# Kernel optimization log

Measured on AMD Instinct MI355X. Metric: run time of the kernel, lower is better.

Reference implementation:

```python
import jax, jax.numpy as jnp
import numpy as np

B, T, C = 4, 2048, 1024
H, D = 16, 64


def setup_inputs() -> dict:
    key = jax.random.key(0)
    ks = jax.random.split(key, 6)
    s = 0.02
    return {
        "x": jax.random.normal(ks[0], (B, T, C), dtype=jnp.float32),
        "wq": jax.random.normal(ks[1], (H, C, D), dtype=jnp.float32) * s,
        "wk": jax.random.normal(ks[2], (H, C, D), dtype=jnp.float32) * s,
        "wv": jax.random.normal(ks[3], (H, C, D), dtype=jnp.float32) * s,
        "w_proj": jax.random.normal(ks[4], (C, C), dtype=jnp.float32) * s,
        "b_proj": jnp.zeros((C,), dtype=jnp.float32),
    }


def reference(x, wq, wk, wv, w_proj, b_proj):
    b, t, c = x.shape
    # per-head projections, vectorized over heads: [B,T,C] x [H,C,D] -> [B,H,T,D]
    q = jnp.einsum("btc,hcd->bhtd", x, wq)
    k = jnp.einsum("btc,hcd->bhtd", x, wk)
    v = jnp.einsum("btc,hcd->bhtd", x, wv)
    # NOTE: original scales by C**-0.5 where C = n_embd (not head_size)
    scale = jnp.asarray(c, x.dtype) ** -0.5
    scores = jnp.einsum("bhtd,bhsd->bhts", q, k) * scale  # [B,H,T,T]
    causal = jnp.tril(jnp.ones((t, t), dtype=bool))
    scores = jnp.where(causal, scores, jnp.finfo(x.dtype).min)
    wei = jax.nn.softmax(scores, axis=-1)
    out = jnp.einsum("bhts,bhsd->bhtd", wei, v)  # [B,H,T,D]
    out = out.transpose(0, 2, 1, 3).reshape(b, t, c)  # concat heads
    return out @ w_proj + b_proj
```

## Files before the change

### kernel.cpp

```cpp
#include <hip/hip_runtime.h>
#include <hip/hip_bf16.h>
#include <stdint.h>

#define B_ 4
#define T_ 2048
#define C_ 1024
#define H_ 16
#define D_ 64

typedef __attribute__((ext_vector_type(8))) short bf16x8;
typedef __attribute__((ext_vector_type(4))) float f32x4;

static __device__ __forceinline__ short f2bf(float f) {
    union { float f; unsigned u; } v; v.f = f;
    unsigned r = v.u + 0x7fffu + ((v.u >> 16) & 1u);
    return (short)(r >> 16);
}

#define GLD_LDS16(g, l) __builtin_amdgcn_global_load_lds( \
    (const __attribute__((address_space(1))) void*)(g),   \
    (__attribute__((address_space(3))) void*)(l), 16, 0, 0)

__global__ void pack_x(const float* __restrict__ x, short* __restrict__ xb) {
    int t = blockIdx.x * blockDim.x + threadIdx.x;
    const float* src = x + (size_t)t * 8;
    float4 v0 = *(const float4*)src;
    float4 v1 = *(const float4*)(src + 4);
    bf16x8 o;
    o[0] = f2bf(v0.x); o[1] = f2bf(v0.y); o[2] = f2bf(v0.z); o[3] = f2bf(v0.w);
    o[4] = f2bf(v1.x); o[5] = f2bf(v1.y); o[6] = f2bf(v1.z); o[7] = f2bf(v1.w);
    *(bf16x8*)(xb + (size_t)t * 8) = o;
}

__global__ void pack_wqkv(const float* __restrict__ wq, const float* __restrict__ wk,
                          const float* __restrict__ wv, short* __restrict__ out) {
    int tid = blockIdx.x * blockDim.x + threadIdx.x;
    int n  = tid >> 7;
    int kc = tid & 127;
    int qkv = n >> 10;
    int h = (n >> 6) & 15;
    int d = n & 63;
    const float* w = (qkv == 0) ? wq : (qkv == 1) ? wk : wv;
    const float* src = w + (size_t)h * (C_ * D_) + d;
    short* dst = out + (size_t)n * C_ + kc * 8;
#pragma unroll
    for (int j = 0; j < 8; ++j)
        dst[j] = f2bf(src[(size_t)(kc * 8 + j) * D_]);
}

__global__ void pack_wproj(const float* __restrict__ wp, short* __restrict__ out) {
    int tid = blockIdx.x * blockDim.x + threadIdx.x;
    int n  = tid >> 7;
    int kc = tid & 127;
    short* dst = out + (size_t)n * C_ + kc * 8;
#pragma unroll
    for (int j = 0; j < 8; ++j)
        dst[j] = f2bf(wp[(size_t)(kc * 8 + j) * C_ + n]);
}

template<bool OUT_F32>
__global__ __launch_bounds__(256)
void gemm_lds(const short* __restrict__ A, const short* __restrict__ Bt,
              void* __restrict__ Cptr, const float* __restrict__ bias,
              int M, int N, int K) {
    __shared__ short As[128 * 32];
    __shared__ short Bs[128 * 32];
    const int tid = threadIdx.x;
    const int lane = tid & 63, wid = tid >> 6;
    const int wr = wid >> 1, wc = wid & 1;
    const int l15 = lane & 15, l4 = lane >> 4;
    const int m0 = blockIdx.y * 128, n0 = blockIdx.x * 128;

    f32x4 acc[4][4] = {};

    for (int k0 = 0; k0 < K; k0 += 32) {
#pragma unroll
        for (int p = 0; p < 2; ++p) {
            int e = p * 256 + tid;
            int r = e >> 2, c = e & 3;
            GLD_LDS16(A  + (size_t)(m0 + r) * K + k0 + c * 8, As + e * 8);
            GLD_LDS16(Bt + (size_t)(n0 + r) * K + k0 + c * 8, Bs + e * 8);
        }
        __syncthreads();
        bf16x8 af[4], bfr[4];
#pragma unroll
        for (int m = 0; m < 4; ++m)
            af[m] = *(const bf16x8*)(As + (wr * 64 + m * 16 + l15) * 32 + l4 * 8);
#pragma unroll
        for (int n = 0; n < 4; ++n)
            bfr[n] = *(const bf16x8*)(Bs + (wc * 64 + n * 16 + l15) * 32 + l4 * 8);
#pragma unroll
        for (int m = 0; m < 4; ++m)
#pragma unroll
            for (int n = 0; n < 4; ++n)
                acc[m][n] = __builtin_amdgcn_mfma_f32_16x16x32_bf16(af[m], bfr[n], acc[m][n], 0, 0, 0);
        __syncthreads();
    }

#pragma unroll
    for (int m = 0; m < 4; ++m) {
        int row_base = m0 + wr * 64 + m * 16 + l4 * 4;
#pragma unroll
        for (int n = 0; n < 4; ++n) {
            int col = n0 + wc * 64 + n * 16 + l15;
#pragma unroll
            for (int r = 0; r < 4; ++r) {
                int row = row_base + r;
                float v = acc[m][n][r];
                if (OUT_F32) {
                    ((float*)Cptr)[(size_t)row * N + col] = v + (bias ? bias[col] : 0.0f);
                } else {
                    ((short*)Cptr)[(size_t)row * N + col] = f2bf(v);
                }
            }
        }
    }
}

__device__ __forceinline__ void softmax_pv_phase1(
    f32x4 S[4], f32x4 O[4], float* mrow, float* srow,
    int qrow0, int s0, bool diag, int l15, int l4, short* ps) {
    float pmax[4];
#pragma unroll
    for (int r = 0; r < 4; ++r) pmax[r] = -1e30f;
#pragma unroll
    for (int n = 0; n < 4; ++n) {
#pragma unroll
        for (int r = 0; r < 4; ++r) {
            float v = S[n][r] * 0.03125f;
            if (diag) {
                int scol = s0 + n * 16 + l15;
                if (scol > qrow0 + r) v = -1e30f;
            }
            S[n][r] = v;
            pmax[r] = fmaxf(pmax[r], v);
        }
    }
#pragma unroll
    for (int r = 0; r < 4; ++r) {
        float v = pmax[r];
        v = fmaxf(v, __shfl_xor(v, 1));
        v = fmaxf(v, __shfl_xor(v, 2));
        v = fmaxf(v, __shfl_xor(v, 4));
        v = fmaxf(v, __shfl_xor(v, 8));
        pmax[r] = v;
    }
    float psum[4];
#pragma unroll
    for (int r = 0; r < 4; ++r) {
        float mnew = fmaxf(mrow[r], pmax[r]);
        float fr = __expf(mrow[r] - mnew);
        mrow[r] = mnew;
        srow[r] *= fr;
#pragma unroll
        for (int n = 0; n < 4; ++n) O[n][r] *= fr;
        psum[r] = 0.0f;
    }
#pragma unroll
    for (int n = 0; n < 4; ++n) {
#pragma unroll
        for (int r = 0; r < 4; ++r) {
            float p = __expf(S[n][r] - mrow[r]);
            psum[r] += p;
            ps[(l4 * 4 + r) * 72 + n * 16 + l15] = f2bf(p);
        }
    }
#pragma unroll
    for (int r = 0; r < 4; ++r) {
        float v = psum[r];
        v += __shfl_xor(v, 1);
        v += __shfl_xor(v, 2);
        v += __shfl_xor(v, 4);
        v += __shfl_xor(v, 8);
        srow[r] += v;
    }
}

__global__ __launch_bounds__(256)
void attn_v5(const short* __restrict__ qkv, short* __restrict__ out) {
    const int pi = blockIdx.x;
    const int bh = blockIdx.y;
    const int b = bh >> 4;
    const int h = bh & 15;
    const int qA0 = pi * 64;
    const int qB0 = (31 - pi) * 64;
    const int ntA = pi + 1;
    const int ntB = 32 - pi;
    const int tid = threadIdx.x;
    const int wave = tid >> 6;
    const int lane = tid & 63;
    const int l15 = lane & 15, l4 = lane >> 4;

    __shared__ short Vt[64][72];
    __shared__ short Ps[4][2][16][72];

    const size_t rs = 3 * C_;
    const short* qbA = qkv + ((size_t)b * T_ + qA0) * rs + h * 64;
    const short* qbB = qkv + ((size_t)b * T_ + qB0) * rs + h * 64;
    const short* kb  = qkv + (size_t)b * T_ * rs + C_ + h * 64;
    const short* vb  = qkv + (size_t)b * T_ * rs + 2 * C_ + h * 64;

    bf16x8 aqA0 = *(const bf16x8*)(qbA + (size_t)(wave * 16 + l15) * rs + l4 * 8);
    bf16x8 aqA1 = *(const bf16x8*)(qbA + (size_t)(wave * 16 + l15) * rs + 32 + l4 * 8);
    bf16x8 aqB0 = *(const bf16x8*)(qbB + (size_t)(wave * 16 + l15) * rs + l4 * 8);
    bf16x8 aqB1 = *(const bf16x8*)(qbB + (size_t)(wave * 16 + l15) * rs + 32 + l4 * 8);

    f32x4 OA[4] = {}, OB[4] = {};
    float mA[4], sA[4], mB[4], sB[4];
#pragma unroll
    for (int r = 0; r < 4; ++r) { mA[r] = mB[r] = -1e30f; sA[r] = sB[r] = 0.0f; }

    short* psB = &Ps[wave][0][0][0];
    short* psA = &Ps[wave][1][0][0];

    for (int t = 0; t < ntB; ++t) {
        const int s0 = t * 64;
        const bool actA = (t < ntA);
        __syncthreads();

#pragma unroll
        for (int p = 0; p < 2; ++p) {
            int e = p * 256 + tid;
            int d = e & 63, sc = e >> 6;
            bf16x8 v;
#pragma unroll
            for (int j = 0; j < 8; ++j)
                v[j] = vb[(size_t)(s0 + sc * 8 + j) * rs + d];
            *(bf16x8*)&Vt[d][sc * 8] = v;
        }

        bf16x8 bk0[4], bk1[4];
#pragma unroll
        for (int n = 0; n < 4; ++n) {
            const short* kr = kb + (size_t)(s0 + n * 16 + l15) * rs;
            bk0[n] = *(const bf16x8*)(kr + l4 * 8);
            bk1[n] = *(const bf16x8*)(kr + 32 + l4 * 8);
        }

        f32x4 S[4];
#pragma unroll
        for (int n = 0; n < 4; ++n) {
            f32x4 z = {};
            z = __builtin_amdgcn_mfma_f32_16x16x32_bf16(aqB0, bk0[n], z, 0, 0, 0);
            S[n] = __builtin_amdgcn_mfma_f32_16x16x32_bf16(aqB1, bk1[n], z, 0, 0, 0);
        }
        softmax_pv_phase1(S, OB, mB, sB, qB0 + wave * 16 + l4 * 4, s0,
                          s0 == qB0, l15, l4, psB);

        if (actA) {
            f32x4 SA[4];
#pragma unroll
            for (int n = 0; n < 4; ++n) {
                f32x4 z = {};
                z = __builtin_amdgcn_mfma_f32_16x16x32_bf16(aqA0, bk0[n], z, 0, 0, 0);
                SA[n] = __builtin_amdgcn_mfma_f32_16x16x32_bf16(aqA1, bk1[n], z, 0, 0, 0);
            }
            softmax_pv_phase1(SA, OA, mA, sA, qA0 + wave * 16 + l4 * 4, s0,
                              s0 == qA0, l15, l4, psA);
        }

        __syncthreads();

        bf16x8 apB0 = *(const bf16x8*)(psB + l15 * 72 + l4 * 8);
        bf16x8 apB1 = *(const bf16x8*)(psB + l15 * 72 + 32 + l4 * 8);
#pragma unroll
        for (int n = 0; n < 4; ++n) {
            bf16x8 bv0 = *(const bf16x8*)&Vt[n * 16 + l15][l4 * 8];
            bf16x8 bv1 = *(const bf16x8*)&Vt[n * 16 + l15][32 + l4 * 8];
            OB[n] = __builtin_amdgcn_mfma_f32_16x16x32_bf16(apB0, bv0, OB[n], 0, 0, 0);
            OB[n] = __builtin_amdgcn_mfma_f32_16x16x32_bf16(apB1, bv1, OB[n], 0, 0, 0);
        }
        if (actA) {
            bf16x8 apA0 = *(const bf16x8*)(psA + l15 * 72 + l4 * 8);
            bf16x8 apA1 = *(const bf16x8*)(psA + l15 * 72 + 32 + l4 * 8);
#pragma unroll
            for (int n = 0; n < 4; ++n) {
                bf16x8 bv0 = *(const bf16x8*)&Vt[n * 16 + l15][l4 * 8];
                bf16x8 bv1 = *(const bf16x8*)&Vt[n * 16 + l15][32 + l4 * 8];
                OA[n] = __builtin_amdgcn_mfma_f32_16x16x32_bf16(apA0, bv0, OA[n], 0, 0, 0);
                OA[n] = __builtin_amdgcn_mfma_f32_16x16x32_bf16(apA1, bv1, OA[n], 0, 0, 0);
            }
        }
    }

#pragma unroll
    for (int r = 0; r < 4; ++r) {
        int rowB = qB0 + wave * 16 + l4 * 4 + r;
        int rowA = qA0 + wave * 16 + l4 * 4 + r;
        float invB = 1.0f / sB[r];
        float invA = 1.0f / sA[r];
        size_t obB = ((size_t)b * T_ + rowB) * C_ + h * 64;
        size_t obA = ((size_t)b * T_ + rowA) * C_ + h * 64;
#pragma unroll
        for (int n = 0; n < 4; ++n) {
            out[obB + n * 16 + l15] = f2bf(OB[n][r] * invB);
            out[obA + n * 16 + l15] = f2bf(OA[n][r] * invA);
        }
    }
}

extern "C" void kernel_launch(void* const* d_in, const int* in_sizes, int n_in,
                              void* d_out, int out_size, void* d_ws, size_t ws_size,
                              hipStream_t stream) {
    const float* x     = (const float*)d_in[0];
    const float* wq    = (const float*)d_in[1];
    const float* wk    = (const float*)d_in[2];
    const float* wv    = (const float*)d_in[3];
    const float* wproj = (const float*)d_in[4];
    const float* bproj = (const float*)d_in[5];
    float* out = (float*)d_out;

    short* wqkv_t  = (short*)d_ws;
    short* wproj_t = wqkv_t + 3072 * 1024;
    short* qkv_b   = wproj_t + 1024 * 1024;
    short* attn_b  = qkv_b + (size_t)8192 * 3072;
    short* xb      = attn_b;

    pack_x<<<4096, 256, 0, stream>>>(x, xb);
    pack_wqkv<<<1536, 256, 0, stream>>>(wq, wk, wv, wqkv_t);
    pack_wproj<<<512, 256, 0, stream>>>(wproj, wproj_t);

    gemm_lds<false><<<dim3(24, 64), 256, 0, stream>>>(
        xb, wqkv_t, qkv_b, nullptr, 8192, 3072, 1024);

    attn_v5<<<dim3(16, 64), 256, 0, stream>>>(qkv_b, attn_b);

    gemm_lds<true><<<dim3(8, 64), 256, 0, stream>>>(
        attn_b, wproj_t, out, bproj, 8192, 1024, 1024);
}
```

Measured before the change: 321.7 us.

## Emit V transposed from QKV GEMM epilogue and drop LDS V staging

The QKV GEMM epilogue now writes Q and K into a 2048-wide buffer and writes V pre-transposed as [B*H, D, T], so the attention kernel can load V fragments directly from global memory into registers. This removes the per-tile scalar strided gather of V into LDS and both block-wide __syncthreads per tile, replacing them with a wave-local lgkmcnt wait since each wave only reads its own P tile. The P buffer row pitch also changes from 72 to 76 to alter LDS bank mapping. The trade-off is a strided transposed store in the GEMM epilogue and more global loads in flight per wave.

New measurement: 371.6 us. +15.5%, slower.

```diff
diff --git a/kernel.cpp b/kernel.cpp
--- a/kernel.cpp
+++ b/kernel.cpp
@@ -9,6 +9,7 @@
 #define D_ 64
 
 typedef __attribute__((ext_vector_type(8))) short bf16x8;
+typedef __attribute__((ext_vector_type(4))) short short4v;
 typedef __attribute__((ext_vector_type(4))) float f32x4;
 
 static __device__ __forceinline__ short f2bf(float f) {
@@ -58,11 +59,11 @@
         dst[j] = f2bf(wp[(size_t)(kc * 8 + j) * C_ + n]);
 }
 
-template<bool OUT_F32>
+template<int MODE>
 __global__ __launch_bounds__(256)
 void gemm_lds(const short* __restrict__ A, const short* __restrict__ Bt,
-              void* __restrict__ Cptr, const float* __restrict__ bias,
-              int M, int N, int K) {
+              void* __restrict__ Cptr, short* __restrict__ vtptr,
+              const float* __restrict__ bias, int M, int N, int K) {
     __shared__ short As[128 * 32];
     __shared__ short Bs[128 * 32];
     const int tid = threadIdx.x;
@@ -103,21 +104,30 @@
 #pragma unroll
         for (int n = 0; n < 4; ++n) {
             int col = n0 + wc * 64 + n * 16 + l15;
-#pragma unroll
-            for (int r = 0; r < 4; ++r) {
-                int row = row_base + r;
-                float v = acc[m][n][r];
-                if (OUT_F32) {
-                    ((float*)Cptr)[(size_t)row * N + col] = v + (bias ? bias[col] : 0.0f);
+            if (MODE == 1) {
+#pragma unroll
+                for (int r = 0; r < 4; ++r)
+                    ((float*)Cptr)[(size_t)(row_base + r) * N + col] =
+                        acc[m][n][r] + bias[col];
+            } else {
+                if (n0 < 2048) {
+#pragma unroll
+                    for (int r = 0; r < 4; ++r)
+                        ((short*)Cptr)[(size_t)(row_base + r) * 2048 + col] = f2bf(acc[m][n][r]);
                 } else {
-                    ((short*)Cptr)[(size_t)row * N + col] = f2bf(v);
+                    int cm = col - 2048;
+                    int bq = row_base >> 11, t = row_base & 2047;
+                    short4v s;
+                    s[0] = f2bf(acc[m][n][0]); s[1] = f2bf(acc[m][n][1]);
+                    s[2] = f2bf(acc[m][n][2]); s[3] = f2bf(acc[m][n][3]);
+                    *(short4v*)(vtptr + ((size_t)bq * 1024 + cm) * 2048 + t) = s;
                 }
             }
         }
     }
 }
 
-__device__ __forceinline__ void softmax_pv_phase1(
+__device__ __forceinline__ void softmax_phase(
     f32x4 S[4], f32x4 O[4], float* mrow, float* srow,
     int qrow0, int s0, bool diag, int l15, int l4, short* ps) {
     float pmax[4];
@@ -162,7 +172,7 @@
         for (int r = 0; r < 4; ++r) {
             float p = __expf(S[n][r] - mrow[r]);
             psum[r] += p;
-            ps[(l4 * 4 + r) * 72 + n * 16 + l15] = f2bf(p);
+            ps[(l4 * 4 + r) * 76 + n * 16 + l15] = f2bf(p);
         }
     }
 #pragma unroll
@@ -177,7 +187,8 @@
 }
 
 __global__ __launch_bounds__(256)
-void attn_v5(const short* __restrict__ qkv, short* __restrict__ out) {
+void attn_v6(const short* __restrict__ qk, const short* __restrict__ vt,
+             short* __restrict__ out) {
     const int pi = blockIdx.x;
     const int bh = blockIdx.y;
     const int b = bh >> 4;
@@ -191,14 +202,13 @@
     const int lane = tid & 63;
     const int l15 = lane & 15, l4 = lane >> 4;
 
-    __shared__ short Vt[64][72];
-    __shared__ short Ps[4][2][16][72];
-
-    const size_t rs = 3 * C_;
-    const short* qbA = qkv + ((size_t)b * T_ + qA0) * rs + h * 64;
-    const short* qbB = qkv + ((size_t)b * T_ + qB0) * rs + h * 64;
-    const short* kb  = qkv + (size_t)b * T_ * rs + C_ + h * 64;
-    const short* vb  = qkv + (size_t)b * T_ * rs + 2 * C_ + h * 64;
+    __shared__ short Ps[4][2][16][76];
+
+    const size_t rs = 2 * C_;
+    const short* qbA = qk + ((size_t)b * T_ + qA0) * rs + h * 64;
+    const short* qbB = qk + ((size_t)b * T_ + qB0) * rs + h * 64;
+    const short* kb  = qk + (size_t)b * T_ * rs + C_ + h * 64;
+    const short* vtb = vt + (size_t)bh * 64 * T_;
 
     bf16x8 aqA0 = *(const bf16x8*)(qbA + (size_t)(wave * 16 + l15) * rs + l4 * 8);
     bf16x8 aqA1 = *(const bf16x8*)(qbA + (size_t)(wave * 16 + l15) * rs + 32 + l4 * 8);
@@ -216,18 +226,6 @@
     for (int t = 0; t < ntB; ++t) {
         const int s0 = t * 64;
         const bool actA = (t < ntA);
-        __syncthreads();
-
-#pragma unroll
-        for (int p = 0; p < 2; ++p) {
-            int e = p * 256 + tid;
-            int d = e & 63, sc = e >> 6;
-            bf16x8 v;
-#pragma unroll
-            for (int j = 0; j < 8; ++j)
-                v[j] = vb[(size_t)(s0 + sc * 8 + j) * rs + d];
-            *(bf16x8*)&Vt[d][sc * 8] = v;
-        }
 
         bf16x8 bk0[4], bk1[4];
 #pragma unroll
@@ -236,6 +234,13 @@
             bk0[n] = *(const bf16x8*)(kr + l4 * 8);
             bk1[n] = *(const bf16x8*)(kr + 32 + l4 * 8);
         }
+        bf16x8 bv0[4], bv1[4];
+#pragma unroll
+        for (int n = 0; n < 4; ++n) {
+            const short* vr = vtb + (size_t)(n * 16 + l15) * T_ + s0;
+            bv0[n] = *(const bf16x8*)(vr + l4 * 8);
+            bv1[n] = *(const bf16x8*)(vr + 32 + l4 * 8);
+        }
 
         f32x4 S[4];
 #pragma unroll
@@ -244,8 +249,8 @@
             z = __builtin_amdgcn_mfma_f32_16x16x32_bf16(aqB0, bk0[n], z, 0, 0, 0);
             S[n] = __builtin_amdgcn_mfma_f32_16x16x32_bf16(aqB1, bk1[n], z, 0, 0, 0);
         }
-        softmax_pv_phase1(S, OB, mB, sB, qB0 + wave * 16 + l4 * 4, s0,
-                          s0 == qB0, l15, l4, psB);
+        softmax_phase(S, OB, mB, sB, qB0 + wave * 16 + l4 * 4, s0, s0 == qB0,
+                      l15, l4, psB);
 
         if (actA) {
             f32x4 SA[4];
@@ -255,30 +260,27 @@
                 z = __builtin_amdgcn_mfma_f32_16x16x32_bf16(aqA0, bk0[n], z, 0, 0, 0);
                 SA[n] = __builtin_amdgcn_mfma_f32_16x16x32_bf16(aqA1, bk1[n], z, 0, 0, 0);
             }
-            softmax_pv_phase1(SA, OA, mA, sA, qA0 + wave * 16 + l4 * 4, s0,
-                              s0 == qA0, l15, l4, psA);
-        }
-
-        __syncthreads();
-
-        bf16x8 apB0 = *(const bf16x8*)(psB + l15 * 72 + l4 * 8);
-        bf16x8 apB1 = *(const bf16x8*)(psB + l15 * 72 + 32 + l4 * 8);
-#pragma unroll
-        for (int n = 0; n < 4; ++n) {
-            bf16x8 bv0 = *(const bf16x8*)&Vt[n * 16 + l15][l4 * 8];
-            bf16x8 bv1 = *(const bf16x8*)&Vt[n * 16 + l15][32 + l4 * 8];
-            OB[n] = __builtin_amdgcn_mfma_f32_16x16x32_bf16(apB0, bv0, OB[n], 0, 0, 0);
-            OB[n] = __builtin_amdgcn_mfma_f32_16x16x32_bf16(apB1, bv1, OB[n], 0, 0, 0);
+            softmax_phase(SA, OA, mA, sA, qA0 + wave * 16 + l4 * 4, s0, s0 == qA0,
+                          l15, l4, psA);
+        }
+
+        asm volatile("s_waitcnt lgkmcnt(0)" ::: "memory");
+        __builtin_amdgcn_sched_barrier(0);
+
+        bf16x8 apB0 = *(const bf16x8*)(psB + l15 * 76 + l4 * 8);
+        bf16x8 apB1 = *(const bf16x8*)(psB + l15 * 76 + 32 + l4 * 8);
+#pragma unroll
+        for (int n = 0; n < 4; ++n) {
+            OB[n] = __builtin_amdgcn_mfma_f32_16x16x32_bf16(apB0, bv0[n], OB[n], 0, 0, 0);
+            OB[n] = __builtin_amdgcn_mfma_f32_16x16x32_bf16(apB1, bv1[n], OB[n], 0, 0, 0);
         }
         if (actA) {
-            bf16x8 apA0 = *(const bf16x8*)(psA + l15 * 72 + l4 * 8);
-            bf16x8 apA1 = *(const bf16x8*)(psA + l15 * 72 + 32 + l4 * 8);
+            bf16x8 apA0 = *(const bf16x8*)(psA + l15 * 76 + l4 * 8);
+            bf16x8 apA1 = *(const bf16x8*)(psA + l15 * 76 + 32 + l4 * 8);
 #pragma unroll
             for (int n = 0; n < 4; ++n) {
-                bf16x8 bv0 = *(const bf16x8*)&Vt[n * 16 + l15][l4 * 8];
-                bf16x8 bv1 = *(const bf16x8*)&Vt[n * 16 + l15][32 + l4 * 8];
-                OA[n] = __builtin_amdgcn_mfma_f32_16x16x32_bf16(apA0, bv0, OA[n], 0, 0, 0);
-                OA[n] = __builtin_amdgcn_mfma_f32_16x16x32_bf16(apA1, bv1, OA[n], 0, 0, 0);
+                OA[n] = __builtin_amdgcn_mfma_f32_16x16x32_bf16(apA0, bv0[n], OA[n], 0, 0, 0);
+                OA[n] = __builtin_amdgcn_mfma_f32_16x16x32_bf16(apA1, bv1[n], OA[n], 0, 0, 0);
             }
         }
     }
@@ -312,19 +314,20 @@
 
     short* wqkv_t  = (short*)d_ws;
     short* wproj_t = wqkv_t + 3072 * 1024;
-    short* qkv_b   = wproj_t + 1024 * 1024;
-    short* attn_b  = qkv_b + (size_t)8192 * 3072;
+    short* qk_b    = wproj_t + 1024 * 1024;
+    short* vt_b    = qk_b + (size_t)8192 * 2048;
+    short* attn_b  = vt_b + (size_t)64 * 64 * 2048;
     short* xb      = attn_b;
 
     pack_x<<<4096, 256, 0, stream>>>(x, xb);
     pack_wqkv<<<1536, 256, 0, stream>>>(wq, wk, wv, wqkv_t);
     pack_wproj<<<512, 256, 0, stream>>>(wproj, wproj_t);
 
-    gemm_lds<false><<<dim3(24, 64), 256, 0, stream>>>(
-        xb, wqkv_t, qkv_b, nullptr, 8192, 3072, 1024);
-
-    attn_v5<<<dim3(16, 64), 256, 0, stream>>>(qkv_b, attn_b);
-
-    gemm_lds<true><<<dim3(8, 64), 256, 0, stream>>>(
-        attn_b, wproj_t, out, bproj, 8192, 1024, 1024);
-}
+    gemm_lds<2><<<dim3(24, 64), 256, 0, stream>>>(
+        xb, wqkv_t, qk_b, vt_b, nullptr, 8192, 3072, 1024);
+
+    attn_v6<<<dim3(16, 64), 256, 0, stream>>>(qk_b, vt_b, attn_b);
+
+    gemm_lds<1><<<dim3(8, 64), 256, 0, stream>>>(
+        attn_b, wproj_t, out, nullptr, bproj, 8192, 1024, 1024);
+}
```

## Double-buffer V tile with register prefetch and drop per-tile P barrier

Applied to the files above, without the earlier changes.

The V tile is now held in two LDS buffers. The next tile's V loads are issued into registers at the start of each iteration and stored into the other buffer after the softmax, so global latency overlaps the QK and softmax compute. Because P is per-wave, the second block barrier becomes a wave-local lgkmcnt wait. The transposed V store uses an XOR swizzle, the P row pitch changes to 76, and MFMA sections are wrapped in s_setprio. This costs more LDS and extra registers for the prefetched V and adds correctness sensitivity to the barrier removal.

Result: slower. 340.3 us (+5.8%).

```diff
diff --git a/kernel.cpp b/kernel.cpp
--- a/kernel.cpp
+++ b/kernel.cpp
@@ -117,7 +117,7 @@
     }
 }
 
-__device__ __forceinline__ void softmax_pv_phase1(
+__device__ __forceinline__ void softmax_phase(
     f32x4 S[4], f32x4 O[4], float* mrow, float* srow,
     int qrow0, int s0, bool diag, int l15, int l4, short* ps) {
     float pmax[4];
@@ -162,7 +162,7 @@
         for (int r = 0; r < 4; ++r) {
             float p = __expf(S[n][r] - mrow[r]);
             psum[r] += p;
-            ps[(l4 * 4 + r) * 72 + n * 16 + l15] = f2bf(p);
+            ps[(l4 * 4 + r) * 76 + n * 16 + l15] = f2bf(p);
         }
     }
 #pragma unroll
@@ -177,7 +177,7 @@
 }
 
 __global__ __launch_bounds__(256)
-void attn_v5(const short* __restrict__ qkv, short* __restrict__ out) {
+void attn_v8(const short* __restrict__ qkv, short* __restrict__ out) {
     const int pi = blockIdx.x;
     const int bh = blockIdx.y;
     const int b = bh >> 4;
@@ -191,8 +191,8 @@
     const int lane = tid & 63;
     const int l15 = lane & 15, l4 = lane >> 4;
 
-    __shared__ short Vt[64][72];
-    __shared__ short Ps[4][2][16][72];
+    __shared__ short Vt[2][64][64];
+    __shared__ short Ps[4][2][16][76];
 
     const size_t rs = 3 * C_;
     const short* qbA = qkv + ((size_t)b * T_ + qA0) * rs + h * 64;
@@ -213,20 +213,34 @@
     short* psB = &Ps[wave][0][0][0];
     short* psA = &Ps[wave][1][0][0];
 
+    const int vd = lane;
+    const int sc0 = wave, sc1 = 4 + wave;
+    const int pc0 = (sc0 ^ (vd & 7)) * 8;
+    const int pc1 = (sc1 ^ (vd & 7)) * 8;
+
+    bf16x8 vreg0, vreg1;
+#pragma unroll
+    for (int j = 0; j < 8; ++j) {
+        vreg0[j] = vb[(size_t)(sc0 * 8 + j) * rs + vd];
+        vreg1[j] = vb[(size_t)(sc1 * 8 + j) * rs + vd];
+    }
+    *(bf16x8*)&Vt[0][vd][pc0] = vreg0;
+    *(bf16x8*)&Vt[0][vd][pc1] = vreg1;
+
     for (int t = 0; t < ntB; ++t) {
         const int s0 = t * 64;
+        const int cur = t & 1;
         const bool actA = (t < ntA);
+        const bool pre = (t + 1 < ntB);
+
         __syncthreads();
 
-#pragma unroll
-        for (int p = 0; p < 2; ++p) {
-            int e = p * 256 + tid;
-            int d = e & 63, sc = e >> 6;
-            bf16x8 v;
-#pragma unroll
-            for (int j = 0; j < 8; ++j)
-                v[j] = vb[(size_t)(s0 + sc * 8 + j) * rs + d];
-            *(bf16x8*)&Vt[d][sc * 8] = v;
+        if (pre) {
+#pragma unroll
+            for (int j = 0; j < 8; ++j) {
+                vreg0[j] = vb[(size_t)(s0 + 64 + sc0 * 8 + j) * rs + vd];
+                vreg1[j] = vb[(size_t)(s0 + 64 + sc1 * 8 + j) * rs + vd];
+            }
         }
 
         bf16x8 bk0[4], bk1[4];
@@ -238,48 +252,64 @@
         }
 
         f32x4 S[4];
+        __builtin_amdgcn_s_setprio(1);
 #pragma unroll
         for (int n = 0; n < 4; ++n) {
             f32x4 z = {};
             z = __builtin_amdgcn_mfma_f32_16x16x32_bf16(aqB0, bk0[n], z, 0, 0, 0);
             S[n] = __builtin_amdgcn_mfma_f32_16x16x32_bf16(aqB1, bk1[n], z, 0, 0, 0);
         }
-        softmax_pv_phase1(S, OB, mB, sB, qB0 + wave * 16 + l4 * 4, s0,
-                          s0 == qB0, l15, l4, psB);
+        __builtin_amdgcn_s_setprio(0);
+        softmax_phase(S, OB, mB, sB, qB0 + wave * 16 + l4 * 4, s0, s0 == qB0,
+                      l15, l4, psB);
 
         if (actA) {
             f32x4 SA[4];
+            __builtin_amdgcn_s_setprio(1);
 #pragma unroll
             for (int n = 0; n < 4; ++n) {
                 f32x4 z = {};
                 z = __builtin_amdgcn_mfma_f32_16x16x32_bf16(aqA0, bk0[n], z, 0, 0, 0);
                 SA[n] = __builtin_amdgcn_mfma_f32_16x16x32_bf16(aqA1, bk1[n], z, 0, 0, 0);
             }
-            softmax_pv_phase1(SA, OA, mA, sA, qA0 + wave * 16 + l4 * 4, s0,
-                              s0 == qA0, l15, l4, psA);
-        }
-
-        __syncthreads();
-
-        bf16x8 apB0 = *(const bf16x8*)(psB + l15 * 72 + l4 * 8);
-        bf16x8 apB1 = *(const bf16x8*)(psB + l15 * 72 + 32 + l4 * 8);
-#pragma unroll
-        for (int n = 0; n < 4; ++n) {
-            bf16x8 bv0 = *(const bf16x8*)&Vt[n * 16 + l15][l4 * 8];
-            bf16x8 bv1 = *(const bf16x8*)&Vt[n * 16 + l15][32 + l4 * 8];
+            __builtin_amdgcn_s_setprio(0);
+            softmax_phase(SA, OA, mA, sA, qA0 + wave * 16 + l4 * 4, s0, s0 == qA0,
+                          l15, l4, psA);
+        }
+
+        if (pre) {
+            *(bf16x8*)&Vt[cur ^ 1][vd][pc0] = vreg0;
+            *(bf16x8*)&Vt[cur ^ 1][vd][pc1] = vreg1;
+        }
+
+        asm volatile("s_waitcnt lgkmcnt(0)" ::: "memory");
+        __builtin_amdgcn_sched_barrier(0);
+
+        bf16x8 apB0 = *(const bf16x8*)(psB + l15 * 76 + l4 * 8);
+        bf16x8 apB1 = *(const bf16x8*)(psB + l15 * 76 + 32 + l4 * 8);
+        __builtin_amdgcn_s_setprio(1);
+#pragma unroll
+        for (int n = 0; n < 4; ++n) {
+            const short* vrow = &Vt[cur][n * 16 + l15][0];
+            bf16x8 bv0 = *(const bf16x8*)(vrow + ((l4 ^ (l15 & 7)) * 8));
+            bf16x8 bv1 = *(const bf16x8*)(vrow + (((l4 + 4) ^ (l15 & 7)) * 8));
             OB[n] = __builtin_amdgcn_mfma_f32_16x16x32_bf16(apB0, bv0, OB[n], 0, 0, 0);
             OB[n] = __builtin_amdgcn_mfma_f32_16x16x32_bf16(apB1, bv1, OB[n], 0, 0, 0);
         }
+        __builtin_amdgcn_s_setprio(0);
         if (actA) {
-            bf16x8 apA0 = *(const bf16x8*)(psA + l15 * 72 + l4 * 8);
-            bf16x8 apA1 = *(const bf16x8*)(psA + l15 * 72 + 32 + l4 * 8);
+            bf16x8 apA0 = *(const bf16x8*)(psA + l15 * 76 + l4 * 8);
+            bf16x8 apA1 = *(const bf16x8*)(psA + l15 * 76 + 32 + l4 * 8);
+            __builtin_amdgcn_s_setprio(1);
 #pragma unroll
             for (int n = 0; n < 4; ++n) {
-                bf16x8 bv0 = *(const bf16x8*)&Vt[n * 16 + l15][l4 * 8];
-                bf16x8 bv1 = *(const bf16x8*)&Vt[n * 16 + l15][32 + l4 * 8];
+                const short* vrow = &Vt[cur][n * 16 + l15][0];
+                bf16x8 bv0 = *(const bf16x8*)(vrow + ((l4 ^ (l15 & 7)) * 8));
+                bf16x8 bv1 = *(const bf16x8*)(vrow + (((l4 + 4) ^ (l15 & 7)) * 8));
                 OA[n] = __builtin_amdgcn_mfma_f32_16x16x32_bf16(apA0, bv0, OA[n], 0, 0, 0);
                 OA[n] = __builtin_amdgcn_mfma_f32_16x16x32_bf16(apA1, bv1, OA[n], 0, 0, 0);
             }
+            __builtin_amdgcn_s_setprio(0);
         }
     }
 
@@ -323,7 +353,7 @@
     gemm_lds<false><<<dim3(24, 64), 256, 0, stream>>>(
         xb, wqkv_t, qkv_b, nullptr, 8192, 3072, 1024);
 
-    attn_v5<<<dim3(16, 64), 256, 0, stream>>>(qkv_b, attn_b);
+    attn_v8<<<dim3(16, 64), 256, 0, stream>>>(qkv_b, attn_b);
 
     gemm_lds<true><<<dim3(8, 64), 256, 0, stream>>>(
         attn_b, wproj_t, out, bproj, 8192, 1024, 1024);
```

## Fold softmax scale into Q projection, use exp2, lazy rescale, swizzle LDS

Applied to the files above, without the earlier changes.

The QKV GEMM epilogue now multiplies the Q columns by scale*log2(e), so the attention kernel can use raw v_exp_f32 (exp2) without a per-score multiply. The online softmax skips the running-max rescale of O and the row sum when the new block maximum stays within 8 units of the stored max across the wave. The Vt LDS tile uses an XOR swizzle in place of padding, and the P tile stride changes from 72 to 76, both aimed at reducing bank conflicts. The lazy rescale lets exponentials reach up to 2^8 before rescaling, which is safe in fp32 but slightly changes the rounding of bf16 P values.

After: 333.3 us. 1.04x slower.

```diff
diff --git a/kernel.cpp b/kernel.cpp
--- a/kernel.cpp
+++ b/kernel.cpp
@@ -17,9 +17,17 @@
     return (short)(r >> 16);
 }
 
+static __device__ __forceinline__ float fast_exp2(float x) {
+    float r;
+    asm("v_exp_f32 %0, %1" : "=v"(r) : "v"(x));
+    return r;
+}
+
 #define GLD_LDS16(g, l) __builtin_amdgcn_global_load_lds( \
     (const __attribute__((address_space(1))) void*)(g),   \
     (__attribute__((address_space(3))) void*)(l), 16, 0, 0)
+
+#define QSCALE 0.04508422f
 
 __global__ void pack_x(const float* __restrict__ x, short* __restrict__ xb) {
     int t = blockIdx.x * blockDim.x + threadIdx.x;
@@ -58,7 +66,7 @@
         dst[j] = f2bf(wp[(size_t)(kc * 8 + j) * C_ + n]);
 }
 
-template<bool OUT_F32>
+template<int MODE>
 __global__ __launch_bounds__(256)
 void gemm_lds(const short* __restrict__ A, const short* __restrict__ Bt,
               void* __restrict__ Cptr, const float* __restrict__ bias,
@@ -107,9 +115,10 @@
             for (int r = 0; r < 4; ++r) {
                 int row = row_base + r;
                 float v = acc[m][n][r];
-                if (OUT_F32) {
-                    ((float*)Cptr)[(size_t)row * N + col] = v + (bias ? bias[col] : 0.0f);
+                if (MODE == 1) {
+                    ((float*)Cptr)[(size_t)row * N + col] = v + bias[col];
                 } else {
+                    if (col < 1024) v *= QSCALE;
                     ((short*)Cptr)[(size_t)row * N + col] = f2bf(v);
                 }
             }
@@ -117,7 +126,7 @@
     }
 }
 
-__device__ __forceinline__ void softmax_pv_phase1(
+__device__ __forceinline__ void softmax_phase(
     f32x4 S[4], f32x4 O[4], float* mrow, float* srow,
     int qrow0, int s0, bool diag, int l15, int l4, short* ps) {
     float pmax[4];
@@ -127,7 +136,7 @@
     for (int n = 0; n < 4; ++n) {
 #pragma unroll
         for (int r = 0; r < 4; ++r) {
-            float v = S[n][r] * 0.03125f;
+            float v = S[n][r];
             if (diag) {
                 int scol = s0 + n * 16 + l15;
                 if (scol > qrow0 + r) v = -1e30f;
@@ -145,24 +154,29 @@
         v = fmaxf(v, __shfl_xor(v, 8));
         pmax[r] = v;
     }
+    int ok = (pmax[0] <= mrow[0] + 8.0f) & (pmax[1] <= mrow[1] + 8.0f) &
+             (pmax[2] <= mrow[2] + 8.0f) & (pmax[3] <= mrow[3] + 8.0f);
+    if (!__all(ok)) {
+#pragma unroll
+        for (int r = 0; r < 4; ++r) {
+            float mnew = fmaxf(mrow[r], pmax[r]);
+            float fr = fast_exp2(mrow[r] - mnew);
+            mrow[r] = mnew;
+            srow[r] *= fr;
+#pragma unroll
+            for (int n = 0; n < 4; ++n) O[n][r] *= fr;
+        }
+    }
     float psum[4];
 #pragma unroll
-    for (int r = 0; r < 4; ++r) {
-        float mnew = fmaxf(mrow[r], pmax[r]);
-        float fr = __expf(mrow[r] - mnew);
-        mrow[r] = mnew;
-        srow[r] *= fr;
-#pragma unroll
-        for (int n = 0; n < 4; ++n) O[n][r] *= fr;
-        psum[r] = 0.0f;
-    }
+    for (int r = 0; r < 4; ++r) psum[r] = 0.0f;
 #pragma unroll
     for (int n = 0; n < 4; ++n) {
 #pragma unroll
         for (int r = 0; r < 4; ++r) {
-            float p = __expf(S[n][r] - mrow[r]);
+            float p = fast_exp2(S[n][r] - mrow[r]);
             psum[r] += p;
-            ps[(l4 * 4 + r) * 72 + n * 16 + l15] = f2bf(p);
+            ps[(l4 * 4 + r) * 76 + n * 16 + l15] = f2bf(p);
         }
     }
 #pragma unroll
@@ -177,7 +191,7 @@
 }
 
 __global__ __launch_bounds__(256)
-void attn_v5(const short* __restrict__ qkv, short* __restrict__ out) {
+void attn_v9(const short* __restrict__ qkv, short* __restrict__ out) {
     const int pi = blockIdx.x;
     const int bh = blockIdx.y;
     const int b = bh >> 4;
@@ -191,8 +205,8 @@
     const int lane = tid & 63;
     const int l15 = lane & 15, l4 = lane >> 4;
 
-    __shared__ short Vt[64][72];
-    __shared__ short Ps[4][2][16][72];
+    __shared__ short Vt[64][64];
+    __shared__ short Ps[4][2][16][76];
 
     const size_t rs = 3 * C_;
     const short* qbA = qkv + ((size_t)b * T_ + qA0) * rs + h * 64;
@@ -226,7 +240,7 @@
 #pragma unroll
             for (int j = 0; j < 8; ++j)
                 v[j] = vb[(size_t)(s0 + sc * 8 + j) * rs + d];
-            *(bf16x8*)&Vt[d][sc * 8] = v;
+            *(bf16x8*)&Vt[d][(sc ^ (d & 7)) * 8] = v;
         }
 
         bf16x8 bk0[4], bk1[4];
@@ -244,8 +258,8 @@
             z = __builtin_amdgcn_mfma_f32_16x16x32_bf16(aqB0, bk0[n], z, 0, 0, 0);
             S[n] = __builtin_amdgcn_mfma_f32_16x16x32_bf16(aqB1, bk1[n], z, 0, 0, 0);
         }
-        softmax_pv_phase1(S, OB, mB, sB, qB0 + wave * 16 + l4 * 4, s0,
-                          s0 == qB0, l15, l4, psB);
+        softmax_phase(S, OB, mB, sB, qB0 + wave * 16 + l4 * 4, s0, s0 == qB0,
+                      l15, l4, psB);
 
         if (actA) {
             f32x4 SA[4];
@@ -255,28 +269,30 @@
                 z = __builtin_amdgcn_mfma_f32_16x16x32_bf16(aqA0, bk0[n], z, 0, 0, 0);
                 SA[n] = __builtin_amdgcn_mfma_f32_16x16x32_bf16(aqA1, bk1[n], z, 0, 0, 0);
             }
-            softmax_pv_phase1(SA, OA, mA, sA, qA0 + wave * 16 + l4 * 4, s0,
-                              s0 == qA0, l15, l4, psA);
+            softmax_phase(SA, OA, mA, sA, qA0 + wave * 16 + l4 * 4, s0, s0 == qA0,
+                          l15, l4, psA);
         }
 
         __syncthreads();
 
-        bf16x8 apB0 = *(const bf16x8*)(psB + l15 * 72 + l4 * 8);
-        bf16x8 apB1 = *(const bf16x8*)(psB + l15 * 72 + 32 + l4 * 8);
-#pragma unroll
-        for (int n = 0; n < 4; ++n) {
-            bf16x8 bv0 = *(const bf16x8*)&Vt[n * 16 + l15][l4 * 8];
-            bf16x8 bv1 = *(const bf16x8*)&Vt[n * 16 + l15][32 + l4 * 8];
+        bf16x8 apB0 = *(const bf16x8*)(psB + l15 * 76 + l4 * 8);
+        bf16x8 apB1 = *(const bf16x8*)(psB + l15 * 76 + 32 + l4 * 8);
+#pragma unroll
+        for (int n = 0; n < 4; ++n) {
+            const short* vrow = &Vt[n * 16 + l15][0];
+            bf16x8 bv0 = *(const bf16x8*)(vrow + ((l4 ^ (l15 & 7)) * 8));
+            bf16x8 bv1 = *(const bf16x8*)(vrow + (((l4 + 4) ^ (l15 & 7)) * 8));
             OB[n] = __builtin_amdgcn_mfma_f32_16x16x32_bf16(apB0, bv0, OB[n], 0, 0, 0);
             OB[n] = __builtin_amdgcn_mfma_f32_16x16x32_bf16(apB1, bv1, OB[n], 0, 0, 0);
         }
         if (actA) {
-            bf16x8 apA0 = *(const bf16x8*)(psA + l15 * 72 + l4 * 8);
-            bf16x8 apA1 = *(const bf16x8*)(psA + l15 * 72 + 32 + l4 * 8);
+            bf16x8 apA0 = *(const bf16x8*)(psA + l15 * 76 + l4 * 8);
+            bf16x8 apA1 = *(const bf16x8*)(psA + l15 * 76 + 32 + l4 * 8);
 #pragma unroll
             for (int n = 0; n < 4; ++n) {
-                bf16x8 bv0 = *(const bf16x8*)&Vt[n * 16 + l15][l4 * 8];
-                bf16x8 bv1 = *(const bf16x8*)&Vt[n * 16 + l15][32 + l4 * 8];
+                const short* vrow = &Vt[n * 16 + l15][0];
+                bf16x8 bv0 = *(const bf16x8*)(vrow + ((l4 ^ (l15 & 7)) * 8));
+                bf16x8 bv1 = *(const bf16x8*)(vrow + (((l4 + 4) ^ (l15 & 7)) * 8));
                 OA[n] = __builtin_amdgcn_mfma_f32_16x16x32_bf16(apA0, bv0, OA[n], 0, 0, 0);
                 OA[n] = __builtin_amdgcn_mfma_f32_16x16x32_bf16(apA1, bv1, OA[n], 0, 0, 0);
             }
@@ -320,11 +336,11 @@
     pack_wqkv<<<1536, 256, 0, stream>>>(wq, wk, wv, wqkv_t);
     pack_wproj<<<512, 256, 0, stream>>>(wproj, wproj_t);
 
-    gemm_lds<false><<<dim3(24, 64), 256, 0, stream>>>(
+    gemm_lds<2><<<dim3(24, 64), 256, 0, stream>>>(
         xb, wqkv_t, qkv_b, nullptr, 8192, 3072, 1024);
 
-    attn_v5<<<dim3(16, 64), 256, 0, stream>>>(qkv_b, attn_b);
-
-    gemm_lds<true><<<dim3(8, 64), 256, 0, stream>>>(
+    attn_v9<<<dim3(16, 64), 256, 0, stream>>>(qkv_b, attn_b);
+
+    gemm_lds<1><<<dim3(8, 64), 256, 0, stream>>>(
         attn_b, wproj_t, out, bproj, 8192, 1024, 1024);
 }
```
